# Kernel optimization log

Measured on AMD Instinct MI355X. Metric: run time of the kernel, lower is better.

Reference implementation:

```python
import jax, jax.numpy as jnp
import numpy as np

B, T, D = 256, 1024, 64          # batch, timesteps, num motor units (input_dim)
H, IC_DIM, F_DIM = 128, 100, 3   # hidden_dim, IC_dim, factors_dim


def setup_inputs() -> dict:
    key = jax.random.key(0)
    ks = jax.random.split(key, 16)
    s = 0.08  # ~1/sqrt(H) scale like torch default init
    f32 = jnp.float32
    return {
        "mu_batch": jax.random.normal(ks[0], (B, T, D), f32),
        # Encoder GRU (input D -> hidden H), PyTorch gate order [r, z, n]
        "We_ih": jax.random.normal(ks[1], (3 * H, D), f32) * s,
        "We_hh": jax.random.normal(ks[2], (3 * H, H), f32) * s,
        "be_ih": jax.random.normal(ks[3], (3 * H,), f32) * s,
        "be_hh": jax.random.normal(ks[4], (3 * H,), f32) * s,
        # IC layer H -> IC_DIM
        "W_ic": jax.random.normal(ks[5], (IC_DIM, H), f32) * s,
        "b_ic": jax.random.normal(ks[6], (IC_DIM,), f32) * s,
        # Generator GRU (input IC_DIM -> hidden H)
        "Wg_ih": jax.random.normal(ks[7], (3 * H, IC_DIM), f32) * s,
        "Wg_hh": jax.random.normal(ks[8], (3 * H, H), f32) * s,
        "bg_ih": jax.random.normal(ks[9], (3 * H,), f32) * s,
        "bg_hh": jax.random.normal(ks[10], (3 * H,), f32) * s,
        # GenToFactors H -> F_DIM
        "W_gf": jax.random.normal(ks[11], (F_DIM, H), f32) * s,
        "b_gf": jax.random.normal(ks[12], (F_DIM,), f32) * s,
        # FactorsToRates F_DIM -> D
        "W_fr": jax.random.normal(ks[13], (D, F_DIM), f32) * s,
        "b_fr": jax.random.normal(ks[14], (D,), f32) * s,
    }


def _gru_step(W_hh, b_hh):
    """PyTorch GRU cell: x_proj = W_ih @ x + b_ih precomputed, gate order r,z,n."""
    def step(h, x_proj):
        gh = h @ W_hh.T + b_hh
        xr, xz, xn = jnp.split(x_proj, 3, axis=-1)
        hr, hz, hn = jnp.split(gh, 3, axis=-1)
        r = jax.nn.sigmoid(xr + hr)
        z = jax.nn.sigmoid(xz + hz)
        n = jnp.tanh(xn + r * hn)
        h_new = (1.0 - z) * n + z * h
        return h_new, h_new
    return step


def reference(mu_batch, We_ih, We_hh, be_ih, be_hh, W_ic, b_ic,
              Wg_ih, Wg_hh, bg_ih, bg_hh, W_gf, b_gf, W_fr, b_fr):
    Bsz, Tlen, _ = mu_batch.shape
    Hdim = We_hh.shape[1]
    h0 = jnp.zeros((Bsz, Hdim), mu_batch.dtype)

    # ----- Encoder GRU: only final hidden state is used -----
    x_proj = jnp.einsum('btd,gd->btg', mu_batch, We_ih) + be_ih   # [B,T,3H]
    h_enc, _ = jax.lax.scan(_gru_step(We_hh, be_hh), h0,
                            jnp.swapaxes(x_proj, 0, 1))           # [B,H]

    # ----- IC layer -----
    IC = h_enc @ W_ic.T + b_ic                                    # [B,IC]

    # ----- Generator GRU: constant input IC fed for T steps, init hidden = h_enc -----
    ic_proj = IC @ Wg_ih.T + bg_ih                                # [B,3H], constant per step
    gstep = _gru_step(Wg_hh, bg_hh)
    def gen_step(h, _):
        return gstep(h, ic_proj)
    _, gen_out = jax.lax.scan(gen_step, h_enc, None, length=Tlen) # [T,B,H]
    gen_out = jnp.swapaxes(gen_out, 0, 1)                         # [B,T,H] == full_gen_out

    # ----- Readout -----
    factors = jnp.einsum('bth,fh->btf', gen_out, W_gf) + b_gf     # [B,T,F]
    rates = jnp.einsum('btf,df->btd', jnp.exp(factors), W_fr) + b_fr  # [B,T,D]
    return rates
```

## Files before the change

### kernel.cpp

```cpp
#include <hip/hip_runtime.h>
#include <hip/hip_bf16.h>

#define Bn 256
#define Tn 1024
#define Dn 64
#define Hn 128
#define G3 384
#define ICn 100
#define BT 16
#define NTH 512
#define LDHE 140
#define LDHG 136
#define LDX 72

typedef _Float16 f16;
typedef __attribute__((ext_vector_type(8))) _Float16 f16x8;
typedef __attribute__((ext_vector_type(4))) _Float16 f16x4;
typedef __attribute__((ext_vector_type(4))) float f32x4;

#define MFMA(a, b, c) __builtin_amdgcn_mfma_f32_16x16x32_f16((a), (b), (c), 0, 0, 0)

#define S_SIG  (-1.4426950408889634f)
#define S_TANH (-2.8853900817779268f)
#define S_EXP  ( 1.4426950408889634f)

__device__ __forceinline__ float rcpa(float x) { return __builtin_amdgcn_rcpf(x); }
__device__ __forceinline__ float ex2(float x) {
#if __has_builtin(__builtin_amdgcn_exp2f)
    return __builtin_amdgcn_exp2f(x);
#else
    return exp2f(x);
#endif
}
__device__ __forceinline__ float sigm2(float x) { return rcpa(1.0f + ex2(x)); }
__device__ __forceinline__ float tanh2(float x) { return fmaf(2.0f, rcpa(1.0f + ex2(x)), -1.0f); }

__device__ __forceinline__ f32x4 splat4(float v) { return (f32x4){v, v, v, v}; }

__device__ __forceinline__ void bar_lds() {
    __builtin_amdgcn_sched_barrier(0);
    asm volatile("s_waitcnt lgkmcnt(0)" ::: "memory");
    __builtin_amdgcn_s_barrier();
    __builtin_amdgcn_sched_barrier(0);
}

__device__ __forceinline__ f16x8 ldw(const float* W, int row, int ldk, int k0, float s) {
    const float* p = W + (size_t)row * ldk + k0;
    f16x8 r;
#pragma unroll
    for (int j = 0; j < 8; ++j) r[j] = (f16)(p[j] * s);
    return r;
}

__global__ __launch_bounds__(NTH, 2)
void enc_kernel(const float* __restrict__ mu,
                const float* __restrict__ We_ih, const float* __restrict__ We_hh,
                const float* __restrict__ be_ih, const float* __restrict__ be_hh,
                float* __restrict__ h_enc)
{
    const int b0 = blockIdx.x * BT;
    const int tid = threadIdx.x;
    const int w = tid >> 6, l = tid & 63, c = l & 15, q = l >> 4;

    __shared__ f16 hbuf[2][BT * LDHE];
    __shared__ f16 xstg[2][8][BT * LDX];

    const int gr = w * 16 + c, gz = Hn + w * 16 + c, gn = 2 * Hn + w * 16 + c;

    f16x8 whf[3][4], wxf[3][2];
#pragma unroll
    for (int kt = 0; kt < 4; ++kt) {
        whf[0][kt] = ldw(We_hh, gr, Hn, kt * 32 + q * 8, S_SIG);
        whf[1][kt] = ldw(We_hh, gz, Hn, kt * 32 + q * 8, S_SIG);
        whf[2][kt] = ldw(We_hh, gn, Hn, kt * 32 + q * 8, S_TANH);
    }
#pragma unroll
    for (int kt = 0; kt < 2; ++kt) {
        wxf[0][kt] = ldw(We_ih, gr, Dn, kt * 32 + q * 8, S_SIG);
        wxf[1][kt] = ldw(We_ih, gz, Dn, kt * 32 + q * 8, S_SIG);
        wxf[2][kt] = ldw(We_ih, gn, Dn, kt * 32 + q * 8, S_TANH);
    }
    const float brc = S_SIG * (be_ih[gr] + be_hh[gr]);
    const float bzc = S_SIG * (be_ih[gz] + be_hh[gz]);
    const float bxn = S_TANH * be_ih[gn];
    const float bhn = S_TANH * be_hh[gn];

    float hreg[4];
#pragma unroll
    for (int r4 = 0; r4 < 4; ++r4) hreg[r4] = 0.0f;
    for (int i = tid; i < BT * Hn; i += NTH) hbuf[0][(i >> 7) * LDHE + (i & 127)] = (f16)0.0f;

    const int SIT = (BT * 8 * Dn) / (NTH * 4);
#pragma unroll
    for (int i = 0; i < SIT; ++i) {
        int f = (i * NTH + tid) * 4;
        int t_off = f >> 10, rem = f & 1023;
        int bb = rem >> 6, d = rem & 63;
        const float4 v = *reinterpret_cast<const float4*>(
            mu + ((size_t)(b0 + bb) * Tn + t_off) * Dn + d);
        f16x4 h4; h4[0] = (f16)v.x; h4[1] = (f16)v.y; h4[2] = (f16)v.z; h4[3] = (f16)v.w;
        *reinterpret_cast<f16x4*>(&xstg[0][t_off][bb * LDX + d]) = h4;
    }
    __syncthreads();

    float4 pre[SIT];
    for (int t = 0; t < Tn; ++t) {
        const int ch = t >> 3, s = t & 7, cur = t & 1, sb = ch & 1;
        if (s == 0 && ch + 1 < Tn / 8) {
#pragma unroll
            for (int i = 0; i < SIT; ++i) {
                int f = (i * NTH + tid) * 4;
                int t_off = f >> 10, rem = f & 1023;
                int bb = rem >> 6, d = rem & 63;
                pre[i] = *reinterpret_cast<const float4*>(
                    mu + ((size_t)(b0 + bb) * Tn + (ch + 1) * 8 + t_off) * Dn + d);
            }
        }
        f16x8 ah[4], ax[2];
#pragma unroll
        for (int kt = 0; kt < 4; ++kt)
            ah[kt] = *reinterpret_cast<const f16x8*>(&hbuf[cur][c * LDHE + kt * 32 + q * 8]);
#pragma unroll
        for (int kt = 0; kt < 2; ++kt)
            ax[kt] = *reinterpret_cast<const f16x8*>(&xstg[sb][s][c * LDX + kt * 32 + q * 8]);

        f32x4 acc0 = splat4(brc), acc1 = splat4(bzc);
        f32x4 acc2 = splat4(bhn), accx = splat4(bxn);
        __builtin_amdgcn_s_setprio(1);
#pragma unroll
        for (int kt = 0; kt < 4; ++kt) {
            acc0 = MFMA(ah[kt], whf[0][kt], acc0);
            acc1 = MFMA(ah[kt], whf[1][kt], acc1);
            acc2 = MFMA(ah[kt], whf[2][kt], acc2);
        }
#pragma unroll
        for (int kt = 0; kt < 2; ++kt) {
            acc0 = MFMA(ax[kt], wxf[0][kt], acc0);
            acc1 = MFMA(ax[kt], wxf[1][kt], acc1);
            accx = MFMA(ax[kt], wxf[2][kt], accx);
        }
        __builtin_amdgcn_s_setprio(0);
#pragma unroll
        for (int r4 = 0; r4 < 4; ++r4) {
            float rg = sigm2(acc0[r4]);
            float zg = sigm2(acc1[r4]);
            float ng = tanh2(fmaf(rg, acc2[r4], accx[r4]));
            float hv = fmaf(zg, hreg[r4] - ng, ng);
            hreg[r4] = hv;
            hbuf[cur ^ 1][(q * 4 + r4) * LDHE + w * 16 + c] = (f16)hv;
        }
        if (s == 7 && ch + 1 < Tn / 8) {
#pragma unroll
            for (int i = 0; i < SIT; ++i) {
                int f = (i * NTH + tid) * 4;
                int t_off = f >> 10, rem = f & 1023;
                int bb = rem >> 6, d = rem & 63;
                f16x4 h4;
                h4[0] = (f16)pre[i].x; h4[1] = (f16)pre[i].y;
                h4[2] = (f16)pre[i].z; h4[3] = (f16)pre[i].w;
                *reinterpret_cast<f16x4*>(&xstg[sb ^ 1][t_off][bb * LDX + d]) = h4;
            }
        }
        bar_lds();
    }
#pragma unroll
    for (int r4 = 0; r4 < 4; ++r4)
        h_enc[(size_t)(b0 + q * 4 + r4) * Hn + w * 16 + c] = hreg[r4];
}

__global__ __launch_bounds__(NTH, 2)
void gen_kernel(const float* __restrict__ h_enc,
                const float* __restrict__ W_ic, const float* __restrict__ b_ic,
                const float* __restrict__ Wg_ih, const float* __restrict__ Wg_hh,
                const float* __restrict__ bg_ih, const float* __restrict__ bg_hh,
                const float* __restrict__ W_gf, const float* __restrict__ b_gf,
                const float* __restrict__ W_fr, const float* __restrict__ b_fr,
                float* __restrict__ out)
{
    const int b0 = blockIdx.x * BT;
    const int tid = threadIdx.x;
    const int w = tid >> 6, l = tid & 63, c = l & 15, q = l >> 4;

    __shared__ f16 hbuf[2][BT * LDHG];
    __shared__ float hencs[BT][Hn];
    __shared__ float ics[BT][ICn];
    __shared__ float xpcs[BT][G3];
    __shared__ float fredB[2][8][BT][4];

    for (int i = tid; i < BT * Hn; i += NTH)
        hencs[i >> 7][i & 127] = h_enc[(size_t)(b0 + (i >> 7)) * Hn + (i & 127)];
    __syncthreads();

    for (int i = tid; i < BT * ICn; i += NTH) {
        int bb = i / ICn, j = i - bb * ICn;
        float a = b_ic[j];
        const float* wr = W_ic + (size_t)j * Hn;
#pragma unroll 4
        for (int k = 0; k < Hn; ++k) a = fmaf(wr[k], hencs[bb][k], a);
        ics[bb][j] = a;
    }
    __syncthreads();

    for (int i = tid; i < BT * G3; i += NTH) {
        int g = i >> 4, bb = i & 15;
        float a = bg_ih[g];
        const float* wr = Wg_ih + (size_t)g * ICn;
#pragma unroll 4
        for (int k = 0; k < ICn; ++k) a = fmaf(wr[k], ics[bb][k], a);
        xpcs[bb][g] = a;
    }
    for (int i = tid; i < BT * Hn; i += NTH)
        hbuf[0][(i >> 7) * LDHG + (i & 127)] = (f16)hencs[i >> 7][i & 127];

    const int gr = w * 16 + c, gz = Hn + w * 16 + c, gn = 2 * Hn + w * 16 + c;

    f16x8 whf[3][4];
#pragma unroll
    for (int kt = 0; kt < 4; ++kt) {
        whf[0][kt] = ldw(Wg_hh, gr, Hn, kt * 32 + q * 8, S_SIG);
        whf[1][kt] = ldw(Wg_hh, gz, Hn, kt * 32 + q * 8, S_SIG);
        whf[2][kt] = ldw(Wg_hh, gn, Hn, kt * 32 + q * 8, S_TANH);
    }
    f16x8 wgff[4];
#pragma unroll
    for (int kt = 0; kt < 4; ++kt) {
        if (c < 3) wgff[kt] = ldw(W_gf, c, Hn, kt * 32 + q * 8, S_EXP);
        else {
            f16x8 z;
#pragma unroll
            for (int j = 0; j < 8; ++j) z[j] = (f16)0.0f;
            wgff[kt] = z;
        }
    }
    const float bgfc = (c < 3) ? S_EXP * b_gf[c] : 0.0f;
    const int d = l;
    const float wfr0 = W_fr[d * 3 + 0], wfr1 = W_fr[d * 3 + 1], wfr2 = W_fr[d * 3 + 2];
    const float bfrd = b_fr[d];
    float* op0 = out + ((size_t)(b0 + w) * Tn) * Dn + d;
    float* op1 = out + ((size_t)(b0 + w + 8) * Tn) * Dn + d;

    float hreg[4];
#pragma unroll
    for (int r4 = 0; r4 < 4; ++r4) hreg[r4] = hencs[q * 4 + r4][w * 16 + c];

    __syncthreads();

    const float bgr = bg_hh[gr], bgz = bg_hh[gz], bhnr = bg_hh[gn];
    f32x4 xrcv, xzcv;
    float xnc[4];
#pragma unroll
    for (int r4 = 0; r4 < 4; ++r4) {
        int bb = q * 4 + r4;
        xrcv[r4] = S_SIG * (xpcs[bb][gr] + bgr);
        xzcv[r4] = S_SIG * (xpcs[bb][gz] + bgz);
        xnc[r4] = S_TANH * xpcs[bb][gn];
    }
    const f32x4 bhnv = splat4(S_TANH * bhnr);
    const f32x4 bgfv = splat4(bgfc);

    auto step = [&](int t, const f16* hb_r, f16* hb_w) {
        const int slot = t & 7, par = (t >> 3) & 1;
        f16x8 ah[4];
#pragma unroll
        for (int kt = 0; kt < 4; ++kt)
            ah[kt] = *reinterpret_cast<const f16x8*>(&hb_r[c * LDHG + kt * 32 + q * 8]);

        f32x4 acc0 = xrcv, acc1 = xzcv, acc2 = bhnv;
        __builtin_amdgcn_s_setprio(1);
#pragma unroll
        for (int kt = 0; kt < 4; ++kt) {
            acc0 = MFMA(ah[kt], whf[0][kt], acc0);
            acc1 = MFMA(ah[kt], whf[1][kt], acc1);
            acc2 = MFMA(ah[kt], whf[2][kt], acc2);
        }
        __builtin_amdgcn_s_setprio(0);
        if (w == slot) {
            f32x4 facc = bgfv;
#pragma unroll
            for (int kt = 0; kt < 4; ++kt) facc = MFMA(ah[kt], wgff[kt], facc);
            if (c < 3) {
#pragma unroll
                for (int r4 = 0; r4 < 4; ++r4)
                    fredB[par][slot][q * 4 + r4][c] = ex2(facc[r4]);
            }
        }
#pragma unroll
        for (int r4 = 0; r4 < 4; ++r4) {
            float rg = sigm2(acc0[r4]);
            float zg = sigm2(acc1[r4]);
            float ng = tanh2(fmaf(rg, acc2[r4], xnc[r4]));
            float hv = fmaf(zg, hreg[r4] - ng, ng);
            hreg[r4] = hv;
            hb_w[(q * 4 + r4) * LDHG + w * 16 + c] = (f16)hv;
        }
        bar_lds();
        if (slot == 7) {
            const int base_row = (t >> 3) * 8 - 1;
#pragma unroll
            for (int s = 0; s < 8; ++s) {
                const int r = base_row + s;
                if (r >= 0) {
                    const float4 f0 = *reinterpret_cast<const float4*>(&fredB[par][s][w][0]);
                    op0[(size_t)r * Dn] = bfrd + f0.x * wfr0 + f0.y * wfr1 + f0.z * wfr2;
                    const float4 f1 = *reinterpret_cast<const float4*>(&fredB[par][s][w + 8][0]);
                    op1[(size_t)r * Dn] = bfrd + f1.x * wfr0 + f1.y * wfr1 + f1.z * wfr2;
                }
            }
        }
    };

    for (int tt = 0; tt < Tn; tt += 2) {
        step(tt,     hbuf[0], hbuf[1]);
        step(tt + 1, hbuf[1], hbuf[0]);
    }
    if (w == 0) {
        f16x8 ah[4];
#pragma unroll
        for (int kt = 0; kt < 4; ++kt)
            ah[kt] = *reinterpret_cast<const f16x8*>(&hbuf[0][c * LDHG + kt * 32 + q * 8]);
        f32x4 facc = bgfv;
#pragma unroll
        for (int kt = 0; kt < 4; ++kt) facc = MFMA(ah[kt], wgff[kt], facc);
        if (c < 3) {
#pragma unroll
            for (int r4 = 0; r4 < 4; ++r4)
                fredB[0][0][q * 4 + r4][c] = ex2(facc[r4]);
        }
    }
    __syncthreads();
    {
        const size_t ofs = (size_t)(Tn - 1) * Dn;
        const float4 f0 = *reinterpret_cast<const float4*>(&fredB[0][0][w][0]);
        op0[ofs] = bfrd + f0.x * wfr0 + f0.y * wfr1 + f0.z * wfr2;
        const float4 f1 = *reinterpret_cast<const float4*>(&fredB[0][0][w + 8][0]);
        op1[ofs] = bfrd + f1.x * wfr0 + f1.y * wfr1 + f1.z * wfr2;
    }
}

extern "C" void kernel_launch(void* const* d_in, const int* in_sizes, int n_in,
                              void* d_out, int out_size, void* d_ws, size_t ws_size,
                              hipStream_t stream) {
    const float* mu    = (const float*)d_in[0];
    const float* We_ih = (const float*)d_in[1];
    const float* We_hh = (const float*)d_in[2];
    const float* be_ih = (const float*)d_in[3];
    const float* be_hh = (const float*)d_in[4];
    const float* W_ic  = (const float*)d_in[5];
    const float* b_ic  = (const float*)d_in[6];
    const float* Wg_ih = (const float*)d_in[7];
    const float* Wg_hh = (const float*)d_in[8];
    const float* bg_ih = (const float*)d_in[9];
    const float* bg_hh = (const float*)d_in[10];
    const float* W_gf  = (const float*)d_in[11];
    const float* b_gf  = (const float*)d_in[12];
    const float* W_fr  = (const float*)d_in[13];
    const float* b_fr  = (const float*)d_in[14];

    float* h_enc = (float*)d_ws;
    float* out = (float*)d_out;

    enc_kernel<<<dim3(Bn / BT), dim3(NTH), 0, stream>>>(mu, We_ih, We_hh, be_ih, be_hh, h_enc);
    gen_kernel<<<dim3(Bn / BT), dim3(NTH), 0, stream>>>(h_enc, W_ic, b_ic, Wg_ih, Wg_hh,
                                                        bg_ih, bg_hh, W_gf, b_gf, W_fr, b_fr, out);
}
```

Measured before the change: 1.401 ms.

## Use 8-slot hidden-state ring to batch readout every 8 steps per wave

Replaces the double-buffered hidden state with an 8-slot LDS ring so that every 8 timesteps each wave computes factors for one past timestep from the ring. Each wave then writes all 16 batch rows for its row with wave-private fredp storage, removing the per-step slot-owner branch and the cross-wave factor reduction buffer. Shared memory is unioned with the setup arrays. An extra barrier is added on every eighth step, and the ring raises LDS footprint, which may affect the two-blocks-per-CU occupancy.

Measured after the change: 1.412 ms. No clear change (+0.7%).

```diff
diff --git a/kernel.cpp b/kernel.cpp
--- a/kernel.cpp
+++ b/kernel.cpp
@@ -12,6 +12,7 @@
 #define LDHE 140
 #define LDHG 136
 #define LDX 72
+#define SLOT (BT * LDHG)
 
 typedef _Float16 f16;
 typedef __attribute__((ext_vector_type(8))) _Float16 f16x8;
@@ -34,7 +35,6 @@
 }
 __device__ __forceinline__ float sigm2(float x) { return rcpa(1.0f + ex2(x)); }
 __device__ __forceinline__ float tanh2(float x) { return fmaf(2.0f, rcpa(1.0f + ex2(x)), -1.0f); }
-
 __device__ __forceinline__ f32x4 splat4(float v) { return (f32x4){v, v, v, v}; }
 
 __device__ __forceinline__ void bar_lds() {
@@ -181,14 +181,15 @@
     const int tid = threadIdx.x;
     const int w = tid >> 6, l = tid & 63, c = l & 15, q = l >> 4;
 
-    __shared__ f16 hbuf[2][BT * LDHG];
-    __shared__ float hencs[BT][Hn];
-    __shared__ float ics[BT][ICn];
-    __shared__ float xpcs[BT][G3];
-    __shared__ float fredB[2][8][BT][4];
+    __shared__ __align__(16) char smem[39424];
+    float* hencs = (float*)smem;
+    float* ics   = hencs + BT * Hn;
+    float* xpcs  = ics + BT * ICn;
+    f16*   ring  = (f16*)smem;
+    float* fredp = (float*)(smem + 8 * SLOT * 2);
 
     for (int i = tid; i < BT * Hn; i += NTH)
-        hencs[i >> 7][i & 127] = h_enc[(size_t)(b0 + (i >> 7)) * Hn + (i & 127)];
+        hencs[(i >> 7) * Hn + (i & 127)] = h_enc[(size_t)(b0 + (i >> 7)) * Hn + (i & 127)];
     __syncthreads();
 
     for (int i = tid; i < BT * ICn; i += NTH) {
@@ -196,8 +197,8 @@
         float a = b_ic[j];
         const float* wr = W_ic + (size_t)j * Hn;
 #pragma unroll 4
-        for (int k = 0; k < Hn; ++k) a = fmaf(wr[k], hencs[bb][k], a);
-        ics[bb][j] = a;
+        for (int k = 0; k < Hn; ++k) a = fmaf(wr[k], hencs[bb * Hn + k], a);
+        ics[bb * ICn + j] = a;
     }
     __syncthreads();
 
@@ -206,11 +207,10 @@
         float a = bg_ih[g];
         const float* wr = Wg_ih + (size_t)g * ICn;
 #pragma unroll 4
-        for (int k = 0; k < ICn; ++k) a = fmaf(wr[k], ics[bb][k], a);
-        xpcs[bb][g] = a;
-    }
-    for (int i = tid; i < BT * Hn; i += NTH)
-        hbuf[0][(i >> 7) * LDHG + (i & 127)] = (f16)hencs[i >> 7][i & 127];
+        for (int k = 0; k < ICn; ++k) a = fmaf(wr[k], ics[bb * ICn + k], a);
+        xpcs[bb * G3 + g] = a;
+    }
+    __syncthreads();
 
     const int gr = w * 16 + c, gz = Hn + w * 16 + c, gn = 2 * Hn + w * 16 + c;
 
@@ -236,14 +236,10 @@
     const int d = l;
     const float wfr0 = W_fr[d * 3 + 0], wfr1 = W_fr[d * 3 + 1], wfr2 = W_fr[d * 3 + 2];
     const float bfrd = b_fr[d];
-    float* op0 = out + ((size_t)(b0 + w) * Tn) * Dn + d;
-    float* op1 = out + ((size_t)(b0 + w + 8) * Tn) * Dn + d;
 
     float hreg[4];
 #pragma unroll
-    for (int r4 = 0; r4 < 4; ++r4) hreg[r4] = hencs[q * 4 + r4][w * 16 + c];
-
-    __syncthreads();
+    for (int r4 = 0; r4 < 4; ++r4) hreg[r4] = hencs[(q * 4 + r4) * Hn + w * 16 + c];
 
     const float bgr = bg_hh[gr], bgz = bg_hh[gz], bhnr = bg_hh[gn];
     f32x4 xrcv, xzcv;
@@ -251,19 +247,25 @@
 #pragma unroll
     for (int r4 = 0; r4 < 4; ++r4) {
         int bb = q * 4 + r4;
-        xrcv[r4] = S_SIG * (xpcs[bb][gr] + bgr);
-        xzcv[r4] = S_SIG * (xpcs[bb][gz] + bgz);
-        xnc[r4] = S_TANH * xpcs[bb][gn];
+        xrcv[r4] = S_SIG * (xpcs[bb * G3 + gr] + bgr);
+        xzcv[r4] = S_SIG * (xpcs[bb * G3 + gz] + bgz);
+        xnc[r4] = S_TANH * xpcs[bb * G3 + gn];
     }
     const f32x4 bhnv = splat4(S_TANH * bhnr);
     const f32x4 bgfv = splat4(bgfc);
 
-    auto step = [&](int t, const f16* hb_r, f16* hb_w) {
-        const int slot = t & 7, par = (t >> 3) & 1;
+    __syncthreads();
+#pragma unroll
+    for (int r4 = 0; r4 < 4; ++r4)
+        ring[(q * 4 + r4) * LDHG + w * 16 + c] = (f16)hreg[r4];
+    __syncthreads();
+
+    for (int t = 0; t < Tn; ++t) {
+        const int s = t & 7;
         f16x8 ah[4];
 #pragma unroll
         for (int kt = 0; kt < 4; ++kt)
-            ah[kt] = *reinterpret_cast<const f16x8*>(&hb_r[c * LDHG + kt * 32 + q * 8]);
+            ah[kt] = *reinterpret_cast<const f16x8*>(&ring[s * SLOT + c * LDHG + kt * 32 + q * 8]);
 
         f32x4 acc0 = xrcv, acc1 = xzcv, acc2 = bhnv;
         __builtin_amdgcn_s_setprio(1);
@@ -274,16 +276,17 @@
             acc2 = MFMA(ah[kt], whf[2][kt], acc2);
         }
         __builtin_amdgcn_s_setprio(0);
-        if (w == slot) {
-            f32x4 facc = bgfv;
-#pragma unroll
-            for (int kt = 0; kt < 4; ++kt) facc = MFMA(ah[kt], wgff[kt], facc);
-            if (c < 3) {
-#pragma unroll
-                for (int r4 = 0; r4 < 4; ++r4)
-                    fredB[par][slot][q * 4 + r4][c] = ex2(facc[r4]);
-            }
-        }
+
+        f32x4 facc = bgfv;
+        if (s == 7) {
+            f16x8 rah[4];
+#pragma unroll
+            for (int kt = 0; kt < 4; ++kt)
+                rah[kt] = *reinterpret_cast<const f16x8*>(&ring[w * SLOT + c * LDHG + kt * 32 + q * 8]);
+#pragma unroll
+            for (int kt = 0; kt < 4; ++kt) facc = MFMA(rah[kt], wgff[kt], facc);
+        }
+
 #pragma unroll
         for (int r4 = 0; r4 < 4; ++r4) {
             float rg = sigm2(acc0[r4]);
@@ -291,49 +294,51 @@
             float ng = tanh2(fmaf(rg, acc2[r4], xnc[r4]));
             float hv = fmaf(zg, hreg[r4] - ng, ng);
             hreg[r4] = hv;
-            hb_w[(q * 4 + r4) * LDHG + w * 16 + c] = (f16)hv;
-        }
+        }
+        if (s == 7) bar_lds();
+#pragma unroll
+        for (int r4 = 0; r4 < 4; ++r4)
+            ring[((t + 1) & 7) * SLOT + (q * 4 + r4) * LDHG + w * 16 + c] = (f16)hreg[r4];
         bar_lds();
-        if (slot == 7) {
-            const int base_row = (t >> 3) * 8 - 1;
-#pragma unroll
-            for (int s = 0; s < 8; ++s) {
-                const int r = base_row + s;
-                if (r >= 0) {
-                    const float4 f0 = *reinterpret_cast<const float4*>(&fredB[par][s][w][0]);
-                    op0[(size_t)r * Dn] = bfrd + f0.x * wfr0 + f0.y * wfr1 + f0.z * wfr2;
-                    const float4 f1 = *reinterpret_cast<const float4*>(&fredB[par][s][w + 8][0]);
-                    op1[(size_t)r * Dn] = bfrd + f1.x * wfr0 + f1.y * wfr1 + f1.z * wfr2;
+
+        if (s == 7) {
+            const int row = t - 8 + w;
+            if (c < 3) {
+#pragma unroll
+                for (int r4 = 0; r4 < 4; ++r4)
+                    fredp[(w * 16 + q * 4 + r4) * 4 + c] = ex2(facc[r4]);
+            }
+            asm volatile("s_waitcnt lgkmcnt(0)" ::: "memory");
+            if (row >= 0) {
+#pragma unroll
+                for (int b = 0; b < BT; ++b) {
+                    const float4 f4 = *reinterpret_cast<const float4*>(&fredp[(w * 16 + b) * 4]);
+                    out[((size_t)(b0 + b) * Tn + row) * Dn + d] =
+                        bfrd + f4.x * wfr0 + f4.y * wfr1 + f4.z * wfr2;
                 }
             }
         }
-    };
-
-    for (int tt = 0; tt < Tn; tt += 2) {
-        step(tt,     hbuf[0], hbuf[1]);
-        step(tt + 1, hbuf[1], hbuf[0]);
     }
     if (w == 0) {
-        f16x8 ah[4];
+        f16x8 rah[4];
 #pragma unroll
         for (int kt = 0; kt < 4; ++kt)
-            ah[kt] = *reinterpret_cast<const f16x8*>(&hbuf[0][c * LDHG + kt * 32 + q * 8]);
+            rah[kt] = *reinterpret_cast<const f16x8*>(&ring[c * LDHG + kt * 32 + q * 8]);
         f32x4 facc = bgfv;
 #pragma unroll
-        for (int kt = 0; kt < 4; ++kt) facc = MFMA(ah[kt], wgff[kt], facc);
+        for (int kt = 0; kt < 4; ++kt) facc = MFMA(rah[kt], wgff[kt], facc);
         if (c < 3) {
 #pragma unroll
             for (int r4 = 0; r4 < 4; ++r4)
-                fredB[0][0][q * 4 + r4][c] = ex2(facc[r4]);
-        }
-    }
-    __syncthreads();
-    {
-        const size_t ofs = (size_t)(Tn - 1) * Dn;
-        const float4 f0 = *reinterpret_cast<const float4*>(&fredB[0][0][w][0]);
-        op0[ofs] = bfrd + f0.x * wfr0 + f0.y * wfr1 + f0.z * wfr2;
-        const float4 f1 = *reinterpret_cast<const float4*>(&fredB[0][0][w + 8][0]);
-        op1[ofs] = bfrd + f1.x * wfr0 + f1.y * wfr1 + f1.z * wfr2;
+                fredp[(q * 4 + r4) * 4 + c] = ex2(facc[r4]);
+        }
+        asm volatile("s_waitcnt lgkmcnt(0)" ::: "memory");
+#pragma unroll
+        for (int b = 0; b < BT; ++b) {
+            const float4 f4 = *reinterpret_cast<const float4*>(&fredp[b * 4]);
+            out[((size_t)(b0 + b) * Tn + (Tn - 1)) * Dn + d] =
+                bfrd + f4.x * wfr0 + f4.y * wfr1 + f4.z * wfr2;
+        }
     }
 }
 
```
